# Performance work log

Hardware: AMD Instinct MI355X
Metric: run time of the kernel (lower is better)

Reference implementation:

```python
import jax, jax.numpy as jnp
import numpy as np

N_A = 50000
N_B = 50000
E = 800000
C_IN = 128
C_OUT = 128


def _lstm_cell_seq1(x, W_ih, b):
    # PyTorch LSTM with seq_len=1 and zero initial state: h = o*tanh(i*g)
    # gate order in weight_ih: [i, f, g, o]; f-gate is unused since c0 = 0.
    gates = x @ W_ih.T + b  # [N, 4H]
    i, f, g, o = jnp.split(gates, 4, axis=-1)
    c = jax.nn.sigmoid(i) * jnp.tanh(g)
    return jax.nn.sigmoid(o) * jnp.tanh(c)


def _conv(x_src, x_dst, edge_index, W_ih, b_lstm, W_lin, b_lin):
    # LSTM message depends only on src features -> compute per node, gather per edge.
    msg = _lstm_cell_seq1(x_src, W_ih, b_lstm)          # [N_src, C_OUT]
    src, dst = edge_index[0], edge_index[1]
    aggr = jax.ops.segment_sum(msg[src], dst, num_segments=x_dst.shape[0])  # [N_dst, C_OUT]
    h = jnp.concatenate([x_dst, aggr], axis=-1)          # [N_dst, C_IN + C_OUT]
    return jax.nn.relu(h @ W_lin.T + b_lin)              # dropout = identity (eval mode)


def setup_inputs() -> dict:
    key = jax.random.key(0)
    ks = jax.random.split(key, 12)
    s = 0.05
    return {
        "x_a": jax.random.normal(ks[0], (N_A, C_IN), jnp.float32),
        "x_b": jax.random.normal(ks[1], (N_B, C_IN), jnp.float32),
        "edge_ab": jax.random.randint(ks[2], (2, E), 0, 50000, jnp.int64 if jax.config.jax_enable_x64 else jnp.int32),
        "edge_ba": jax.random.randint(ks[3], (2, E), 0, 50000, jnp.int64 if jax.config.jax_enable_x64 else jnp.int32),
        "W_ih_ab": jax.random.normal(ks[4], (4 * C_OUT, C_IN), jnp.float32) * s,
        "b_ab": jax.random.normal(ks[5], (4 * C_OUT,), jnp.float32) * s,
        "W_lin_ab": jax.random.normal(ks[6], (C_OUT, C_IN + C_OUT), jnp.float32) * s,
        "b_lin_ab": jax.random.normal(ks[7], (C_OUT,), jnp.float32) * s,
        "W_ih_ba": jax.random.normal(ks[8], (4 * C_OUT, C_IN), jnp.float32) * s,
        "b_ba": jax.random.normal(ks[9], (4 * C_OUT,), jnp.float32) * s,
        "W_lin_ba": jax.random.normal(ks[10], (C_OUT, C_IN + C_OUT), jnp.float32) * s,
        "b_lin_ba": jax.random.normal(ks[11], (C_OUT,), jnp.float32) * s,
    }


def reference(x_a, x_b, edge_ab, edge_ba,
              W_ih_ab, b_ab, W_lin_ab, b_lin_ab,
              W_ih_ba, b_ba, W_lin_ba, b_lin_ba):
    # a_to_b relation updates type_b nodes; b_to_a updates type_a nodes.
    out_b = _conv(x_a, x_b, edge_ab, W_ih_ab, b_ab, W_lin_ab, b_lin_ab)
    out_a = _conv(x_b, x_a, edge_ba, W_ih_ba, b_ba, W_lin_ba, b_lin_ba)
    # stack (same shapes) => [2, N, C_OUT]: index 0 = new x_a, index 1 = new x_b
    return jnp.stack([out_a, out_b], axis=0)
```

## Files before the change

### kernel.cpp

```cpp
#include <hip/hip_runtime.h>
#include <cstdint>
#include <cstddef>

#define CCH 128
#define TK 4096
#define FCAP 5120
#define SLOT 5120
#define MAXBKT 512
#define XPAD 136
#define APAD 264

typedef __attribute__((ext_vector_type(8))) short short8;
typedef __attribute__((ext_vector_type(4))) float floatx4;

__device__ __forceinline__ unsigned short f2bf(float f) {
    unsigned u = __builtin_bit_cast(unsigned, f);
    u += 0x7fffu + ((u >> 16) & 1u);
    return (unsigned short)(u >> 16);
}
__device__ __forceinline__ float bf2f(unsigned short h) {
    unsigned u = ((unsigned)h) << 16;
    return __builtin_bit_cast(float, u);
}
__device__ __forceinline__ float sigmoidf_(float x) { return 1.0f / (1.0f + __expf(-x)); }
__device__ __forceinline__ float tanh_fast(float x) {
    x = fminf(fmaxf(x, -10.0f), 10.0f);
    float e = __expf(2.0f * x);
    return (e - 1.0f) / (e + 1.0f);
}

__global__ __launch_bounds__(256) void prep_weights_kernel(
    const float* __restrict__ Wih0, const float* __restrict__ Wih1,
    const float* __restrict__ Wlin0, const float* __restrict__ Wlin1,
    unsigned short* __restrict__ frag_ih, unsigned short* __restrict__ frag_lin)
{
    int t = blockIdx.x * 256 + threadIdx.x;
    if (t < 12288) {
        int l  = t & 63;
        int kc = (t >> 6) & 3;
        int ct = (t >> 8) & 7;
        int g  = (t >> 11) % 3;
        int rel = t / 6144;
        int gb = (g == 0) ? 0 : (g == 1 ? 256 : 384);
        const float* W = rel ? Wih1 : Wih0;
        int n  = gb + ct * 16 + (l & 15);
        int kb = kc * 32 + (l >> 4) * 8;
        unsigned short* o = frag_ih + (size_t)t * 8;
#pragma unroll
        for (int j = 0; j < 8; j++) o[j] = f2bf(W[(size_t)n * CCH + kb + j]);
    } else {
        int t2 = t - 12288;
        if (t2 >= 8192) return;
        int l  = t2 & 63;
        int kc = (t2 >> 6) & 7;
        int ct = (t2 >> 9) & 7;
        int rel = t2 >> 12;
        const float* W = rel ? Wlin1 : Wlin0;
        int n  = ct * 16 + (l & 15);
        int kb = kc * 32 + (l >> 4) * 8;
        unsigned short* o = frag_lin + (size_t)t2 * 8;
#pragma unroll
        for (int j = 0; j < 8; j++) o[j] = f2bf(W[(size_t)n * 256 + kb + j]);
    }
}

__global__ __launch_bounds__(256) void lstm_hist_kernel(
    const float* __restrict__ x0, const float* __restrict__ x1,
    const unsigned short* __restrict__ wfrag,
    const float* __restrict__ b0, const float* __restrict__ b1,
    unsigned short* __restrict__ msg0, unsigned short* __restrict__ msg1,
    int N0, int N1, int nblk0,
    const int* __restrict__ dstE0, const int* __restrict__ dstE1,
    int* __restrict__ H, int E0, int E1, int nbkt0, int NBKT, int nT)
{
    __shared__ unsigned short xs[32 * XPAD];
    __shared__ int h[MAXBKT];
    const int tid = threadIdx.x;

    if (blockIdx.x < nT) {
        for (int i = tid; i < NBKT; i += 256) h[i] = 0;
        __syncthreads();
        const long long Etot = (long long)E0 + E1;
        const long long base = (long long)blockIdx.x * TK;
        for (int i = tid; i < TK; i += 256) {
            long long e = base + i;
            if (e >= Etot) break;
            int g;
            if (e < E0) g = dstE0[e] >> 8;
            else        g = nbkt0 + (dstE1[e - E0] >> 8);
            atomicAdd(&h[g], 1);
        }
        __syncthreads();
        int* row = H + (size_t)blockIdx.x * NBKT;
        for (int i = tid; i < NBKT; i += 256) row[i] = h[i];
        return;
    }

    const int lb = blockIdx.x - nT;
    const int rel = (lb >= nblk0);
    const int nb = (rel ? (lb - nblk0) : lb) * 32;
    const float* x = rel ? x1 : x0;
    const float* bias = rel ? b1 : b0;
    unsigned short* msg = rel ? msg1 : msg0;
    const int N = rel ? N1 : N0;
    const unsigned short* wf = wfrag + (size_t)rel * 6144 * 8;

    {
        int r = tid >> 3;
        int c0 = (tid & 7) * 16;
        int n = nb + r;
        unsigned short* dstp = xs + r * XPAD + c0;
        if (n < N) {
            const float4* srcp = (const float4*)(x + (size_t)n * CCH + c0);
#pragma unroll
            for (int qq = 0; qq < 4; qq++) {
                float4 v = srcp[qq];
                unsigned u0 = (unsigned)f2bf(v.x) | ((unsigned)f2bf(v.y) << 16);
                unsigned u1 = (unsigned)f2bf(v.z) | ((unsigned)f2bf(v.w) << 16);
                *(uint2*)(dstp + qq * 4) = make_uint2(u0, u1);
            }
        } else {
#pragma unroll
            for (int qq = 0; qq < 4; qq++) *(uint2*)(dstp + qq * 4) = make_uint2(0u, 0u);
        }
    }
    __syncthreads();

    const int w = tid >> 6;
    const int l = tid & 63;
    const int ctb2 = w * 2;
    const int q = l >> 4;
    const int m16 = l & 15;

    floatx4 acc[3][2][2];
#pragma unroll
    for (int g = 0; g < 3; g++)
#pragma unroll
        for (int c = 0; c < 2; c++)
#pragma unroll
            for (int mt = 0; mt < 2; mt++) acc[g][c][mt] = (floatx4){0.f, 0.f, 0.f, 0.f};

    const unsigned short* arow0 = xs + m16 * XPAD + q * 8;
    const unsigned short* arow1 = xs + (16 + m16) * XPAD + q * 8;
#pragma unroll
    for (int kc = 0; kc < 4; kc++) {
        short8 af0 = *(const short8*)(arow0 + kc * 32);
        short8 af1 = *(const short8*)(arow1 + kc * 32);
#pragma unroll
        for (int g = 0; g < 3; g++)
#pragma unroll
            for (int c = 0; c < 2; c++) {
                const unsigned short* bp = wf + ((((size_t)g * 8 + (ctb2 + c)) * 4 + kc) * 64 + l) * 8;
                short8 bv = *(const short8*)bp;
                acc[g][c][0] = __builtin_amdgcn_mfma_f32_16x16x32_bf16(af0, bv, acc[g][c][0], 0, 0, 0);
                acc[g][c][1] = __builtin_amdgcn_mfma_f32_16x16x32_bf16(af1, bv, acc[g][c][1], 0, 0, 0);
            }
    }

    __syncthreads();
#pragma unroll
    for (int c = 0; c < 2; c++) {
        const int col = (ctb2 + c) * 16 + m16;
        const float bi = bias[col], bg = bias[256 + col], bo = bias[384 + col];
#pragma unroll
        for (int mt = 0; mt < 2; mt++)
#pragma unroll
            for (int r = 0; r < 4; r++) {
                const int nl = mt * 16 + q * 4 + r;
                float iv = sigmoidf_(acc[0][c][mt][r] + bi);
                float gv = tanh_fast(acc[1][c][mt][r] + bg);
                float ov = sigmoidf_(acc[2][c][mt][r] + bo);
                xs[nl * XPAD + col] = f2bf(ov * tanh_fast(iv * gv));
            }
    }
    __syncthreads();
    {
        int r = tid >> 3;
        int c0 = (tid & 7) * 16;
        int n = nb + r;
        if (n < N) {
            const unsigned short* srow = xs + r * XPAD + c0;
            uint4 v0 = *(const uint4*)(srow);
            uint4 v1 = *(const uint4*)(srow + 8);
            unsigned short* drow = msg + (size_t)n * CCH + c0;
            *(uint4*)(drow) = v0;
            *(uint4*)(drow + 8) = v1;
        }
    }
}

__global__ __launch_bounds__(256) void colscan_kernel(
    int* __restrict__ H, int* __restrict__ btot, int nT, int NBKT)
{
    __shared__ int s[256];
    __shared__ int carry;
    const int g = blockIdx.x;
    const int tid = threadIdx.x;
    if (tid == 0) carry = 0;
    __syncthreads();
    for (int base = 0; base < nT; base += 256) {
        int b = base + tid;
        int v = (b < nT) ? H[(size_t)b * NBKT + g] : 0;
        s[tid] = v;
        __syncthreads();
#pragma unroll
        for (int off = 1; off < 256; off <<= 1) {
            int t = (tid >= off) ? s[tid - off] : 0;
            __syncthreads();
            s[tid] += t;
            __syncthreads();
        }
        if (b < nT) H[(size_t)b * NBKT + g] = s[tid] - v + carry;
        __syncthreads();
        if (tid == 255) carry += s[255];
        __syncthreads();
    }
    if (tid == 0) btot[g] = carry;
}

__global__ __launch_bounds__(256) void tile_scatter_kernel(
    const int* __restrict__ src0, const int* __restrict__ dst0,
    const int* __restrict__ src1, const int* __restrict__ dst1,
    const int* __restrict__ H,
    unsigned* __restrict__ packed, int E0, int E1, int nbkt0, int NBKT)
{
    __shared__ int cur[MAXBKT];
    const int tid = threadIdx.x;
    const int* row = H + (size_t)blockIdx.x * NBKT;
    for (int i = tid; i < NBKT; i += 256) cur[i] = i * SLOT + row[i];
    __syncthreads();
    const long long Etot = (long long)E0 + E1;
    const long long base = (long long)blockIdx.x * TK;
    for (int i = tid; i < TK; i += 256) {
        long long e = base + i;
        if (e >= Etot) break;
        int s, g, k;
        if (e < E0) { int d = dst0[e]; s = src0[e]; g = d >> 8; k = d & 255; }
        else { long long ee = e - E0; int d = dst1[ee]; s = src1[ee]; g = nbkt0 + (d >> 8); k = d & 255; }
        int pos = atomicAdd(&cur[g], 1);
        packed[pos] = ((unsigned)k << 24) | (unsigned)s;
    }
}

__global__ __launch_bounds__(256) void fine_sort_kernel(
    unsigned* __restrict__ packed, const int* __restrict__ btot,
    int* __restrict__ offs0, int* __restrict__ deg0,
    int* __restrict__ offs1, int* __restrict__ deg1,
    int N0, int N1, int nbkt0)
{
    __shared__ unsigned pin[FCAP];
    __shared__ int hist[256], scn[256], cur[256];
    const int g = blockIdx.x;
    const int tid = threadIdx.x;
    const int base = g * SLOT;
    const int cnt = min(btot[g], FCAP);

    for (int i = tid; i < cnt; i += 256) pin[i] = packed[base + i];
    hist[tid] = 0;
    __syncthreads();
    for (int i = tid; i < cnt; i += 256) atomicAdd(&hist[pin[i] >> 24], 1);
    __syncthreads();
    int v = hist[tid];
    scn[tid] = v;
    __syncthreads();
#pragma unroll
    for (int off = 1; off < 256; off <<= 1) {
        int t = (tid >= off) ? scn[tid - off] : 0;
        __syncthreads();
        scn[tid] += t;
        __syncthreads();
    }
    int excl = scn[tid] - v;
    cur[tid] = excl;
    {
        const int rel = (g >= nbkt0);
        const int lb = rel ? g - nbkt0 : g;
        const int n = lb * 256 + tid;
        const int N = rel ? N1 : N0;
        if (n < N) {
            if (rel) { offs1[n] = base + excl; deg1[n] = v; }
            else     { offs0[n] = base + excl; deg0[n] = v; }
        }
    }
    __syncthreads();
    int* op = (int*)packed;
    for (int i = tid; i < cnt; i += 256) {
        unsigned p = pin[i];
        int pos = atomicAdd(&cur[p >> 24], 1);
        op[base + pos] = (int)(p & 0x00FFFFFFu);
    }
}

__global__ __launch_bounds__(512) void gather_linear_kernel(
    const float* __restrict__ xd0, const float* __restrict__ xd1,
    const unsigned short* __restrict__ msg0, const unsigned short* __restrict__ msg1,
    const int* __restrict__ csr,
    const int* __restrict__ offs0, const int* __restrict__ offs1,
    const int* __restrict__ deg0, const int* __restrict__ deg1,
    const unsigned short* __restrict__ wfrag,
    const float* __restrict__ bl0, const float* __restrict__ bl1,
    float* __restrict__ out0, float* __restrict__ out1,
    int P0, int P1, int N0, int N1)
{
    __shared__ unsigned short s[32 * APAD];
    const int tid = threadIdx.x;
    const int grp = blockIdx.x >> 3;
    const int sub = blockIdx.x & 7;
    const int rel = (sub >> 2) & 1;
    const int lb = grp * 4 + (sub & 3);
    const int P = rel ? P1 : P0;
    if (lb >= P) return;
    const int nb = lb * 32;
    const float* xd = rel ? xd1 : xd0;
    const unsigned short* msg = rel ? msg1 : msg0;
    const int* offs = rel ? offs1 : offs0;
    const int* deg = rel ? deg1 : deg0;
    const float* bl = rel ? bl1 : bl0;
    float* outp = rel ? out1 : out0;
    const int N = rel ? N1 : N0;
    const unsigned short* wf = wfrag + (size_t)rel * 4096 * 8;

    {
        int r = tid >> 4;
        int c0 = (tid & 15) * 8;
        int n = nb + r;
        unsigned short* drow = s + r * APAD + c0;
        if (n < N) {
            const floatx4* srcp = (const floatx4*)(xd + (size_t)n * CCH + c0);
            floatx4 v0 = __builtin_nontemporal_load(srcp);
            floatx4 v1 = __builtin_nontemporal_load(srcp + 1);
            uint4 u;
            u.x = (unsigned)f2bf(v0[0]) | ((unsigned)f2bf(v0[1]) << 16);
            u.y = (unsigned)f2bf(v0[2]) | ((unsigned)f2bf(v0[3]) << 16);
            u.z = (unsigned)f2bf(v1[0]) | ((unsigned)f2bf(v1[1]) << 16);
            u.w = (unsigned)f2bf(v1[2]) | ((unsigned)f2bf(v1[3]) << 16);
            *(uint4*)drow = u;
        } else {
            *(uint4*)drow = make_uint4(0u, 0u, 0u, 0u);
        }
    }
    {
        const int w = tid >> 6;
        const int l = tid & 63;
        const int g = l >> 4;
        const int c = l & 15;
        const int nloc = w * 4 + g;
        const int n = nb + nloc;
        float a0 = 0.f, a1 = 0.f, a2 = 0.f, a3 = 0.f;
        float a4 = 0.f, a5 = 0.f, a6 = 0.f, a7 = 0.f;
        if (n < N) {
            const int start = offs[n];
            const int cnt = deg[n];
            const int* ce = csr + start;
            const unsigned short* mb = msg + c * 8;
#define ACC8(U) { \
            a0 += bf2f((unsigned short)(U.x)); a1 += bf2f((unsigned short)((U.x) >> 16)); \
            a2 += bf2f((unsigned short)(U.y)); a3 += bf2f((unsigned short)((U.y) >> 16)); \
            a4 += bf2f((unsigned short)(U.z)); a5 += bf2f((unsigned short)((U.z) >> 16)); \
            a6 += bf2f((unsigned short)(U.w)); a7 += bf2f((unsigned short)((U.w) >> 16)); }
            int j = 0;
            for (; j + 4 <= cnt; j += 4) {
                int s0 = ce[j], s1 = ce[j + 1], s2 = ce[j + 2], s3 = ce[j + 3];
                uint4 u0 = *(const uint4*)(mb + (size_t)s0 * CCH);
                uint4 u1 = *(const uint4*)(mb + (size_t)s1 * CCH);
                uint4 u2 = *(const uint4*)(mb + (size_t)s2 * CCH);
                uint4 u3 = *(const uint4*)(mb + (size_t)s3 * CCH);
                ACC8(u0); ACC8(u1); ACC8(u2); ACC8(u3);
            }
            for (; j < cnt; j++) {
                uint4 u0 = *(const uint4*)(mb + (size_t)ce[j] * CCH);
                ACC8(u0);
            }
#undef ACC8
        }
        uint4 o;
        o.x = (unsigned)f2bf(a0) | ((unsigned)f2bf(a1) << 16);
        o.y = (unsigned)f2bf(a2) | ((unsigned)f2bf(a3) << 16);
        o.z = (unsigned)f2bf(a4) | ((unsigned)f2bf(a5) << 16);
        o.w = (unsigned)f2bf(a6) | ((unsigned)f2bf(a7) << 16);
        *(uint4*)(s + nloc * APAD + CCH + c * 8) = o;
    }
    __syncthreads();

    const int w = tid >> 6;
    const int l = tid & 63;
    const int q = l >> 4;
    const int m16 = l & 15;

    floatx4 acc[2];
    acc[0] = (floatx4){0.f, 0.f, 0.f, 0.f};
    acc[1] = (floatx4){0.f, 0.f, 0.f, 0.f};

    const unsigned short* arow0 = s + m16 * APAD + q * 8;
    const unsigned short* arow1 = s + (16 + m16) * APAD + q * 8;
#pragma unroll
    for (int kc = 0; kc < 8; kc++) {
        short8 af0 = *(const short8*)(arow0 + kc * 32);
        short8 af1 = *(const short8*)(arow1 + kc * 32);
        const unsigned short* bp = wf + ((((size_t)w) * 8 + kc) * 64 + l) * 8;
        short8 bv = *(const short8*)bp;
        acc[0] = __builtin_amdgcn_mfma_f32_16x16x32_bf16(af0, bv, acc[0], 0, 0, 0);
        acc[1] = __builtin_amdgcn_mfma_f32_16x16x32_bf16(af1, bv, acc[1], 0, 0, 0);
    }

    const int col = w * 16 + m16;
    const float bv = bl[col];
#pragma unroll
    for (int mt = 0; mt < 2; mt++)
#pragma unroll
        for (int r = 0; r < 4; r++) {
            const int node = nb + mt * 16 + q * 4 + r;
            if (node < N) {
                float v = fmaxf(acc[mt][r] + bv, 0.0f);
                __builtin_nontemporal_store(v, &outp[(size_t)node * CCH + col]);
            }
        }
}

extern "C" void kernel_launch(void* const* d_in, const int* in_sizes, int n_in,
                              void* d_out, int out_size, void* d_ws, size_t ws_size,
                              hipStream_t stream) {
    const float* x_a      = (const float*)d_in[0];
    const float* x_b      = (const float*)d_in[1];
    const int*   e_ab     = (const int*)d_in[2];
    const int*   e_ba     = (const int*)d_in[3];
    const float* W_ih_ab  = (const float*)d_in[4];
    const float* b_ab     = (const float*)d_in[5];
    const float* W_lin_ab = (const float*)d_in[6];
    const float* b_lin_ab = (const float*)d_in[7];
    const float* W_ih_ba  = (const float*)d_in[8];
    const float* b_ba     = (const float*)d_in[9];
    const float* W_lin_ba = (const float*)d_in[10];
    const float* b_lin_ba = (const float*)d_in[11];

    const int NA = in_sizes[0] / CCH;
    const int NB = in_sizes[1] / CCH;
    const int E0 = in_sizes[2] / 2;
    const int E1 = in_sizes[3] / 2;

    float* out = (float*)d_out;
    char* ws = (char*)d_ws;
    size_t off = 0;
    auto alloc = [&](size_t bytes) { char* p = ws + off; off += (bytes + 255) & ~(size_t)255; return p; };

    unsigned short* wfrag_ih  = (unsigned short*)alloc(12288 * 8 * 2);
    unsigned short* wfrag_lin = (unsigned short*)alloc(8192 * 8 * 2);
    unsigned short* msg_a     = (unsigned short*)alloc((size_t)NA * CCH * 2);
    unsigned short* msg_b     = (unsigned short*)alloc((size_t)NB * CCH * 2);

    const int nbkt0 = (NB + 255) / 256;
    const int nbkt1 = (NA + 255) / 256;
    const int NBKT = nbkt0 + nbkt1;
    const long long Etot = (long long)E0 + E1;
    const int nT = (int)((Etot + TK - 1) / TK);

    int* H      = (int*)alloc((size_t)nT * NBKT * 4);
    int* btot   = (int*)alloc((size_t)NBKT * 4);
    int* offs_b = (int*)alloc((size_t)NB * 4);
    int* offs_a = (int*)alloc((size_t)NA * 4);
    int* deg_b  = (int*)alloc((size_t)NB * 4);
    int* deg_a  = (int*)alloc((size_t)NA * 4);
    unsigned* packed = (unsigned*)alloc((size_t)NBKT * SLOT * 4);

    const int nblkA = (NA + 31) / 32;
    const int nblkB = (NB + 31) / 32;

    prep_weights_kernel<<<80, 256, 0, stream>>>(
        W_ih_ab, W_ih_ba, W_lin_ab, W_lin_ba, wfrag_ih, wfrag_lin);

    lstm_hist_kernel<<<nT + nblkA + nblkB, 256, 0, stream>>>(
        x_a, x_b, wfrag_ih, b_ab, b_ba, msg_a, msg_b, NA, NB, nblkA,
        e_ab + E0, e_ba + E1, H, E0, E1, nbkt0, NBKT, nT);

    colscan_kernel<<<NBKT, 256, 0, stream>>>(H, btot, nT, NBKT);
    tile_scatter_kernel<<<nT, 256, 0, stream>>>(
        e_ab, e_ab + E0, e_ba, e_ba + E1, H, packed, E0, E1, nbkt0, NBKT);
    fine_sort_kernel<<<NBKT, 256, 0, stream>>>(
        packed, btot, offs_b, deg_b, offs_a, deg_a, NB, NA, nbkt0);

    const int Pmax = (nblkB > nblkA) ? nblkB : nblkA;
    const int G = ((Pmax + 3) / 4) * 8;
    gather_linear_kernel<<<G, 512, 0, stream>>>(
        x_b, x_a, msg_a, msg_b, (const int*)packed,
        offs_b, offs_a, deg_b, deg_a, wfrag_lin, b_lin_ab, b_lin_ba,
        out + (size_t)NA * CCH, out, nblkB, nblkA, NB, NA);
}
```

Baseline: 263.7 us.

## Replace histogram+column-scan with per-tile atomic bucket reservation in scatter

Removes the separate per-tile histogram pass and the column-scan kernel. Each scatter block now builds its local bucket histogram and reserves space in each coarse bucket with one global atomicAdd per bucket, and btot is zeroed inside the weight-prep kernel. This drops a kernel launch, the H matrix traffic and the serial scan, at the cost of a non-deterministic order of edges within a bucket, which the fine sort must tolerate. The final output store also changes from nontemporal to a regular store.

```diff
diff --git a/kernel.cpp b/kernel.cpp
--- a/kernel.cpp
+++ b/kernel.cpp
@@ -32,7 +32,8 @@
 __global__ __launch_bounds__(256) void prep_weights_kernel(
     const float* __restrict__ Wih0, const float* __restrict__ Wih1,
     const float* __restrict__ Wlin0, const float* __restrict__ Wlin1,
-    unsigned short* __restrict__ frag_ih, unsigned short* __restrict__ frag_lin)
+    unsigned short* __restrict__ frag_ih, unsigned short* __restrict__ frag_lin,
+    int* __restrict__ btot, int NBKT)
 {
     int t = blockIdx.x * 256 + threadIdx.x;
     if (t < 12288) {
@@ -48,9 +49,8 @@
         unsigned short* o = frag_ih + (size_t)t * 8;
 #pragma unroll
         for (int j = 0; j < 8; j++) o[j] = f2bf(W[(size_t)n * CCH + kb + j]);
-    } else {
+    } else if (t < 20480) {
         int t2 = t - 12288;
-        if (t2 >= 8192) return;
         int l  = t2 & 63;
         int kc = (t2 >> 6) & 7;
         int ct = (t2 >> 9) & 7;
@@ -61,42 +61,23 @@
         unsigned short* o = frag_lin + (size_t)t2 * 8;
 #pragma unroll
         for (int j = 0; j < 8; j++) o[j] = f2bf(W[(size_t)n * 256 + kb + j]);
-    }
-}
-
-__global__ __launch_bounds__(256) void lstm_hist_kernel(
+    } else {
+        int z = t - 20480;
+        if (z < NBKT) btot[z] = 0;
+    }
+}
+
+__global__ __launch_bounds__(256) void lstm_kernel(
     const float* __restrict__ x0, const float* __restrict__ x1,
     const unsigned short* __restrict__ wfrag,
     const float* __restrict__ b0, const float* __restrict__ b1,
     unsigned short* __restrict__ msg0, unsigned short* __restrict__ msg1,
-    int N0, int N1, int nblk0,
-    const int* __restrict__ dstE0, const int* __restrict__ dstE1,
-    int* __restrict__ H, int E0, int E1, int nbkt0, int NBKT, int nT)
+    int N0, int N1, int nblk0)
 {
     __shared__ unsigned short xs[32 * XPAD];
-    __shared__ int h[MAXBKT];
     const int tid = threadIdx.x;
 
-    if (blockIdx.x < nT) {
-        for (int i = tid; i < NBKT; i += 256) h[i] = 0;
-        __syncthreads();
-        const long long Etot = (long long)E0 + E1;
-        const long long base = (long long)blockIdx.x * TK;
-        for (int i = tid; i < TK; i += 256) {
-            long long e = base + i;
-            if (e >= Etot) break;
-            int g;
-            if (e < E0) g = dstE0[e] >> 8;
-            else        g = nbkt0 + (dstE1[e - E0] >> 8);
-            atomicAdd(&h[g], 1);
-        }
-        __syncthreads();
-        int* row = H + (size_t)blockIdx.x * NBKT;
-        for (int i = tid; i < NBKT; i += 256) row[i] = h[i];
-        return;
-    }
-
-    const int lb = blockIdx.x - nT;
+    const int lb = blockIdx.x;
     const int rel = (lb >= nblk0);
     const int nb = (rel ? (lb - nblk0) : lb) * 32;
     const float* x = rel ? x1 : x0;
@@ -189,48 +170,33 @@
     }
 }
 
-__global__ __launch_bounds__(256) void colscan_kernel(
-    int* __restrict__ H, int* __restrict__ btot, int nT, int NBKT)
-{
-    __shared__ int s[256];
-    __shared__ int carry;
-    const int g = blockIdx.x;
-    const int tid = threadIdx.x;
-    if (tid == 0) carry = 0;
-    __syncthreads();
-    for (int base = 0; base < nT; base += 256) {
-        int b = base + tid;
-        int v = (b < nT) ? H[(size_t)b * NBKT + g] : 0;
-        s[tid] = v;
-        __syncthreads();
-#pragma unroll
-        for (int off = 1; off < 256; off <<= 1) {
-            int t = (tid >= off) ? s[tid - off] : 0;
-            __syncthreads();
-            s[tid] += t;
-            __syncthreads();
-        }
-        if (b < nT) H[(size_t)b * NBKT + g] = s[tid] - v + carry;
-        __syncthreads();
-        if (tid == 255) carry += s[255];
-        __syncthreads();
-    }
-    if (tid == 0) btot[g] = carry;
-}
-
 __global__ __launch_bounds__(256) void tile_scatter_kernel(
     const int* __restrict__ src0, const int* __restrict__ dst0,
     const int* __restrict__ src1, const int* __restrict__ dst1,
-    const int* __restrict__ H,
+    int* __restrict__ btot,
     unsigned* __restrict__ packed, int E0, int E1, int nbkt0, int NBKT)
 {
+    __shared__ int h[MAXBKT];
     __shared__ int cur[MAXBKT];
     const int tid = threadIdx.x;
-    const int* row = H + (size_t)blockIdx.x * NBKT;
-    for (int i = tid; i < NBKT; i += 256) cur[i] = i * SLOT + row[i];
+    for (int i = tid; i < NBKT; i += 256) h[i] = 0;
     __syncthreads();
     const long long Etot = (long long)E0 + E1;
     const long long base = (long long)blockIdx.x * TK;
+    for (int i = tid; i < TK; i += 256) {
+        long long e = base + i;
+        if (e >= Etot) break;
+        int g;
+        if (e < E0) g = dst0[e] >> 8;
+        else        g = nbkt0 + (dst1[e - E0] >> 8);
+        atomicAdd(&h[g], 1);
+    }
+    __syncthreads();
+    for (int i = tid; i < NBKT; i += 256) {
+        int c = h[i];
+        cur[i] = i * SLOT + (c ? atomicAdd(&btot[i], c) : 0);
+    }
+    __syncthreads();
     for (int i = tid; i < TK; i += 256) {
         long long e = base + i;
         if (e >= Etot) break;
@@ -410,10 +376,7 @@
 #pragma unroll
         for (int r = 0; r < 4; r++) {
             const int node = nb + mt * 16 + q * 4 + r;
-            if (node < N) {
-                float v = fmaxf(acc[mt][r] + bv, 0.0f);
-                __builtin_nontemporal_store(v, &outp[(size_t)node * CCH + col]);
-            }
+            if (node < N) outp[(size_t)node * CCH + col] = fmaxf(acc[mt][r] + bv, 0.0f);
         }
 }
 
@@ -454,7 +417,6 @@
     const long long Etot = (long long)E0 + E1;
     const int nT = (int)((Etot + TK - 1) / TK);
 
-    int* H      = (int*)alloc((size_t)nT * NBKT * 4);
     int* btot   = (int*)alloc((size_t)NBKT * 4);
     int* offs_b = (int*)alloc((size_t)NB * 4);
     int* offs_a = (int*)alloc((size_t)NA * 4);
@@ -465,16 +427,14 @@
     const int nblkA = (NA + 31) / 32;
     const int nblkB = (NB + 31) / 32;
 
-    prep_weights_kernel<<<80, 256, 0, stream>>>(
-        W_ih_ab, W_ih_ba, W_lin_ab, W_lin_ba, wfrag_ih, wfrag_lin);
-
-    lstm_hist_kernel<<<nT + nblkA + nblkB, 256, 0, stream>>>(
-        x_a, x_b, wfrag_ih, b_ab, b_ba, msg_a, msg_b, NA, NB, nblkA,
-        e_ab + E0, e_ba + E1, H, E0, E1, nbkt0, NBKT, nT);
-
-    colscan_kernel<<<NBKT, 256, 0, stream>>>(H, btot, nT, NBKT);
+    prep_weights_kernel<<<82, 256, 0, stream>>>(
+        W_ih_ab, W_ih_ba, W_lin_ab, W_lin_ba, wfrag_ih, wfrag_lin, btot, NBKT);
+
+    lstm_kernel<<<nblkA + nblkB, 256, 0, stream>>>(
+        x_a, x_b, wfrag_ih, b_ab, b_ba, msg_a, msg_b, NA, NB, nblkA);
+
     tile_scatter_kernel<<<nT, 256, 0, stream>>>(
-        e_ab, e_ab + E0, e_ba, e_ba + E1, H, packed, E0, E1, nbkt0, NBKT);
+        e_ab, e_ab + E0, e_ba, e_ba + E1, btot, packed, E0, E1, nbkt0, NBKT);
     fine_sort_kernel<<<NBKT, 256, 0, stream>>>(
         packed, btot, offs_b, deg_b, offs_a, deg_a, NB, NA, nbkt0);
 
```

Result: slower. 269.4 us (+2.1%).
